# Kernel optimization log

Hardware: AMD Instinct MI355X
Metric: run time of the kernel (lower is better)

Reference implementation:

```python
import jax, jax.numpy as jnp
import numpy as np


def _dependence(X):
    # X: [N, D]. dom[i, j] = True iff X[i, d] > X[j, d] for all d.
    # Diagonal is automatically False (X[i] > X[i] is all False), matching the
    # original's explicit i != j exclusion.
    dom = jnp.all(X[:, None, :] > X[None, :, :], axis=-1)  # [N, N] bool
    n = X.shape[0]
    Z = dom.sum(axis=1).astype(X.dtype) / (n - 1)  # [N]
    return Z


def setup_inputs() -> dict:
    key = jax.random.key(0)
    k1, k2 = jax.random.split(key)
    N, D = 8192, 8
    X = jax.random.normal(k1, (N, D), dtype=jnp.float32)
    X_hat = jax.random.normal(k2, (N, D), dtype=jnp.float32)
    return {"X": X, "X_hat": X_hat}


def reference(X, X_hat):
    Z = jnp.sort(_dependence(X))
    Zhat = jnp.sort(_dependence(X_hat))
    return jnp.sum(jnp.abs(Z - Zhat)) / Z.shape[0]
```

## Files before the change

### kernel.cpp

```cpp
#include <hip/hip_runtime.h>

constexpr int N = 8192;
constexpr int D = 8;
constexpr int BLK = 256;
constexpr int JTILE = 512;
constexpr int JCH = N / JTILE;

__global__ __launch_bounds__(BLK) void dom_count_kernel(
    const float* __restrict__ X, const float* __restrict__ Xh,
    int* __restrict__ counts) {
  const float* M = (blockIdx.z == 0) ? X : Xh;
  int* cnt_out = counts + blockIdx.z * N;

  __shared__ float4 tile[JTILE * 2];

  const int tid = threadIdx.x;
  const int i = blockIdx.x * BLK + tid;

  const float4* Mi = reinterpret_cast<const float4*>(M + (size_t)i * D);
  const float4 r0 = Mi[0];
  const float4 r1 = Mi[1];

  const int j0 = blockIdx.y * JTILE;
  const float4* src = reinterpret_cast<const float4*>(M + (size_t)j0 * D);
  for (int k = tid; k < JTILE * 2; k += BLK) tile[k] = src[k];
  __syncthreads();

  int cnt = 0;
#pragma unroll 4
  for (int j = 0; j < JTILE; ++j) {
    const float4 a = tile[2 * j];
    const float4 b = tile[2 * j + 1];
    const int ok = (r0.x > a.x) & (r0.y > a.y) & (r0.z > a.z) & (r0.w > a.w) &
                   (r1.x > b.x) & (r1.y > b.y) & (r1.z > b.z) & (r1.w > b.w);
    cnt += ok;
  }
  atomicAdd(&cnt_out[i], cnt);
}

__global__ __launch_bounds__(1024) void finalize_kernel(
    const int* __restrict__ counts, float* __restrict__ out) {
  __shared__ int hist[N];
  __shared__ int ssum[1024];
  __shared__ int total;

  const int tid = threadIdx.x;
  for (int k = tid; k < N; k += 1024) hist[k] = 0;
  if (tid == 0) total = 0;
  __syncthreads();

  for (int k = tid; k < N; k += 1024) {
    atomicAdd(&hist[counts[k]], 1);
    atomicAdd(&hist[counts[N + k]], -1);
  }
  __syncthreads();

  int local[8];
  int s = 0;
#pragma unroll
  for (int q = 0; q < 8; ++q) {
    local[q] = hist[tid * 8 + q];
    s += local[q];
  }

  ssum[tid] = s;
  __syncthreads();
  for (int off = 1; off < 1024; off <<= 1) {
    const int v = (tid >= off) ? ssum[tid - off] : 0;
    __syncthreads();
    ssum[tid] += v;
    __syncthreads();
  }

  int run = ssum[tid] - s;
  int acc = 0;
#pragma unroll
  for (int q = 0; q < 8; ++q) {
    run += local[q];
    acc += (run < 0) ? -run : run;
  }
  atomicAdd(&total, acc);
  __syncthreads();

  if (tid == 0) {
    out[0] = (float)((double)total / ((double)(N - 1) * (double)N));
  }
}

extern "C" void kernel_launch(void* const* d_in, const int* in_sizes, int n_in,
                              void* d_out, int out_size, void* d_ws, size_t ws_size,
                              hipStream_t stream) {
  const float* X = (const float*)d_in[0];
  const float* Xh = (const float*)d_in[1];
  float* out = (float*)d_out;
  int* counts = (int*)d_ws;

  hipMemsetAsync(counts, 0, 2 * N * sizeof(int), stream);

  dim3 grid(N / BLK, JCH, 2);
  dom_count_kernel<<<grid, BLK, 0, stream>>>(X, Xh, counts);
  finalize_kernel<<<1, 1024, 0, stream>>>(counts, out);
}
```

Baseline: 116.7 us.

## Register-block four rows per thread, use min-of-differences test, and shuffle-based scan

Each thread now keeps four i-rows in registers and reuses every shared-memory j-row across all four, which cuts LDS traffic per comparison. The eight-way comparison becomes a tree of fminf over differences with a single compare. JTILE is halved to keep the grid size reasonable. The finalize kernel swaps its barrier-heavy shared-memory scan and atomic total for wavefront shuffles. The risks are higher register pressure and a subtle change for ties or NaN (subtraction could underflow to zero for very close values).

```diff
diff --git a/kernel.cpp b/kernel.cpp
--- a/kernel.cpp
+++ b/kernel.cpp
@@ -1,9 +1,10 @@
 #include <hip/hip_runtime.h>
 
 constexpr int N = 8192;
-constexpr int D = 8;
 constexpr int BLK = 256;
-constexpr int JTILE = 512;
+constexpr int IPT = 4;
+constexpr int ITILE = BLK * IPT;
+constexpr int JTILE = 256;
 constexpr int JCH = N / JTILE;
 
 __global__ __launch_bounds__(BLK) void dom_count_kernel(
@@ -15,38 +16,51 @@
   __shared__ float4 tile[JTILE * 2];
 
   const int tid = threadIdx.x;
-  const int i = blockIdx.x * BLK + tid;
-
-  const float4* Mi = reinterpret_cast<const float4*>(M + (size_t)i * D);
-  const float4 r0 = Mi[0];
-  const float4 r1 = Mi[1];
+  const int ibase = blockIdx.x * ITILE + tid;
 
   const int j0 = blockIdx.y * JTILE;
-  const float4* src = reinterpret_cast<const float4*>(M + (size_t)j0 * D);
+  const float4* src = reinterpret_cast<const float4*>(M + (size_t)j0 * 8);
   for (int k = tid; k < JTILE * 2; k += BLK) tile[k] = src[k];
+
+  float4 r0[IPT], r1[IPT];
+#pragma unroll
+  for (int p = 0; p < IPT; ++p) {
+    const float4* Mi = reinterpret_cast<const float4*>(M + (size_t)(ibase + p * BLK) * 8);
+    r0[p] = Mi[0];
+    r1[p] = Mi[1];
+  }
   __syncthreads();
 
-  int cnt = 0;
-#pragma unroll 4
+  int cnt[IPT] = {};
+#pragma unroll 2
   for (int j = 0; j < JTILE; ++j) {
     const float4 a = tile[2 * j];
     const float4 b = tile[2 * j + 1];
-    const int ok = (r0.x > a.x) & (r0.y > a.y) & (r0.z > a.z) & (r0.w > a.w) &
-                   (r1.x > b.x) & (r1.y > b.y) & (r1.z > b.z) & (r1.w > b.w);
-    cnt += ok;
+#pragma unroll
+    for (int p = 0; p < IPT; ++p) {
+      const float m0 = fminf(fminf(r0[p].x - a.x, r0[p].y - a.y),
+                             fminf(r0[p].z - a.z, r0[p].w - a.w));
+      const float m1 = fminf(fminf(r1[p].x - b.x, r1[p].y - b.y),
+                             fminf(r1[p].z - b.z, r1[p].w - b.w));
+      cnt[p] += (fminf(m0, m1) > 0.0f) ? 1 : 0;
+    }
   }
-  atomicAdd(&cnt_out[i], cnt);
+#pragma unroll
+  for (int p = 0; p < IPT; ++p) atomicAdd(&cnt_out[ibase + p * BLK], cnt[p]);
 }
 
 __global__ __launch_bounds__(1024) void finalize_kernel(
     const int* __restrict__ counts, float* __restrict__ out) {
   __shared__ int hist[N];
-  __shared__ int ssum[1024];
-  __shared__ int total;
+  __shared__ int wsum[16];
+  __shared__ int wexc[16];
+  __shared__ int wabs[16];
 
   const int tid = threadIdx.x;
+  const int lane = tid & 63;
+  const int wid = tid >> 6;
+
   for (int k = tid; k < N; k += 1024) hist[k] = 0;
-  if (tid == 0) total = 0;
   __syncthreads();
 
   for (int k = tid; k < N; k += 1024) {
@@ -63,26 +77,39 @@
     s += local[q];
   }
 
-  ssum[tid] = s;
+  int incl = s;
+#pragma unroll
+  for (int off = 1; off < 64; off <<= 1) {
+    const int v = __shfl_up(incl, off);
+    if (lane >= off) incl += v;
+  }
+  if (lane == 63) wsum[wid] = incl;
   __syncthreads();
-  for (int off = 1; off < 1024; off <<= 1) {
-    const int v = (tid >= off) ? ssum[tid - off] : 0;
-    __syncthreads();
-    ssum[tid] += v;
-    __syncthreads();
+
+  if (tid == 0) {
+    int acc = 0;
+#pragma unroll
+    for (int w = 0; w < 16; ++w) { wexc[w] = acc; acc += wsum[w]; }
   }
+  __syncthreads();
 
-  int run = ssum[tid] - s;
+  int run = wexc[wid] + (incl - s);
   int acc = 0;
 #pragma unroll
   for (int q = 0; q < 8; ++q) {
     run += local[q];
     acc += (run < 0) ? -run : run;
   }
-  atomicAdd(&total, acc);
+
+#pragma unroll
+  for (int off = 32; off > 0; off >>= 1) acc += __shfl_down(acc, off);
+  if (lane == 0) wabs[wid] = acc;
   __syncthreads();
 
   if (tid == 0) {
+    int total = 0;
+#pragma unroll
+    for (int w = 0; w < 16; ++w) total += wabs[w];
     out[0] = (float)((double)total / ((double)(N - 1) * (double)N));
   }
 }
@@ -97,7 +124,7 @@
 
   hipMemsetAsync(counts, 0, 2 * N * sizeof(int), stream);
 
-  dim3 grid(N / BLK, JCH, 2);
+  dim3 grid(N / ITILE, JCH, 2);
   dom_count_kernel<<<grid, BLK, 0, stream>>>(X, Xh, counts);
   finalize_kernel<<<1, 1024, 0, stream>>>(counts, out);
 }
```

After: 110.9 us. 5.0% less time.
